# Optimization experiments

Hardware: AMD Instinct MI355X
Metric: run time of the kernel (lower is better)

## Reference

```python
import jax, jax.numpy as jnp
import numpy as np

H = 2048      # hidden_size
NH = 16       # num heads
HD = H // NH  # head_dim = 128


def setup_inputs() -> dict:
    key = jax.random.key(0)
    ks = jax.random.split(key, 5)
    x = jax.random.normal(ks[0], (2, 2048, H), dtype=jnp.float32)
    # qkv_proj: Linear(H, 3H) with bias; out_proj: Linear(H, H) with bias
    s = 1.0 / np.sqrt(H)
    w_qkv = jax.random.uniform(ks[1], (3 * H, H), jnp.float32, -s, s)
    b_qkv = jax.random.uniform(ks[2], (3 * H,), jnp.float32, -s, s)
    w_out = jax.random.uniform(ks[3], (H, H), jnp.float32, -s, s)
    b_out = jax.random.uniform(ks[4], (H,), jnp.float32, -s, s)
    return {"x": x, "w_qkv": w_qkv, "b_qkv": b_qkv, "w_out": w_out, "b_out": b_out}


def reference(x, w_qkv, b_qkv, w_out, b_out):
    b, s, _ = x.shape
    # fused QKV projection: [b, s, 3H]
    xqkv = jnp.einsum('bsh,oh->bso', x, w_qkv) + b_qkv
    xqkv = xqkv.reshape(b, s, 3, NH, HD)
    q = xqkv[:, :, 0].transpose(0, 2, 1, 3)  # [b, nh, s, hd]
    k = xqkv[:, :, 1].transpose(0, 2, 1, 3)
    v = xqkv[:, :, 2].transpose(0, 2, 1, 3)
    # non-causal SDPA (attn_mask=None, is_causal=False)
    scores = jnp.einsum('bhqd,bhkd->bhqk', q, k) / np.sqrt(HD).astype(np.float32)
    attn = jax.nn.softmax(scores, axis=-1)
    out = jnp.einsum('bhqk,bhkd->bhqd', attn, v)
    out = out.transpose(0, 2, 1, 3).reshape(b, s, NH * HD)
    return jnp.einsum('bsh,oh->bso', out, w_out) + b_out
```

## Files before the change

### kernel.cpp

```cpp
#include <hip/hip_runtime.h>
#include <hip/hip_bf16.h>


typedef __bf16 bf16x8 __attribute__((ext_vector_type(8)));
typedef float f32x4 __attribute__((ext_vector_type(4)));
typedef unsigned short ushort8_t __attribute__((ext_vector_type(8)));
typedef unsigned short ushort4_t __attribute__((ext_vector_type(4)));

__device__ __forceinline__ unsigned short f2bf(float f) {
  unsigned int u = __float_as_uint(f);
  u += 0x7fffu + ((u >> 16) & 1u);
  return (unsigned short)(u >> 16);
}

__device__ __forceinline__ unsigned int pk2bf(float lo, float hi) {
  unsigned int a = (__float_as_uint(lo) + 0x8000u) >> 16;
  unsigned int b = (__float_as_uint(hi) + 0x8000u) & 0xffff0000u;
  return a | b;
}

__device__ __forceinline__ float fexp2(float x) {
#if __has_builtin(__builtin_amdgcn_exp2f)
  return __builtin_amdgcn_exp2f(x);
#else
  return exp2f(x);
#endif
}

__device__ __forceinline__ f32x4 mfma16(bf16x8 a, bf16x8 b, f32x4 c) {
  return __builtin_amdgcn_mfma_f32_16x16x32_bf16(a, b, c, 0, 0, 0);
}

__device__ __forceinline__ void gload_lds16(const void* g, void* lds) {
  __builtin_amdgcn_global_load_lds(
      (const __attribute__((address_space(1))) unsigned int*)g,
      (__attribute__((address_space(3))) unsigned int*)lds, 16, 0, 0);
}

__global__ __launch_bounds__(256) void f32_to_bf16_k(const float* __restrict__ in,
                                                     unsigned short* __restrict__ out,
                                                     int n) {
  int i = (blockIdx.x * 256 + threadIdx.x) * 8;
  if (i >= n) return;
  float4 a = *(const float4*)(in + i);
  float4 b = *(const float4*)(in + i + 4);
  ushort8_t o;
  o[0] = f2bf(a.x); o[1] = f2bf(a.y); o[2] = f2bf(a.z); o[3] = f2bf(a.w);
  o[4] = f2bf(b.x); o[5] = f2bf(b.y); o[6] = f2bf(b.z); o[7] = f2bf(b.w);
  *(ushort8_t*)(out + i) = o;
}

template <int BF16OUT>
__global__ __launch_bounds__(256) void gemm_nt(const unsigned short* __restrict__ A,
                                               const unsigned short* __restrict__ B,
                                               const float* __restrict__ bias,
                                               void* __restrict__ Cout,
                                               int M, int N, int K) {
  __shared__ __attribute__((aligned(16))) unsigned short As[128 * 64];
  __shared__ __attribute__((aligned(16))) unsigned short Bs[128 * 64];
  const int tid = threadIdx.x;
  const int lane = tid & 63;
  const int wv = tid >> 6;
  const int wm = wv >> 1, wn = wv & 1;
  const int lr = lane & 15, lg = lane >> 4;
  const int m0 = blockIdx.y * 128, n0 = blockIdx.x * 128;

  f32x4 acc[4][4];
#pragma unroll
  for (int i = 0; i < 4; ++i)
#pragma unroll
    for (int j = 0; j < 4; ++j) acc[i][j] = (f32x4){0.f, 0.f, 0.f, 0.f};

  for (int kt = 0; kt < K; kt += 64) {
    __syncthreads();
#pragma unroll
    for (int i = 0; i < 4; ++i) {
      int c = i * 256 + tid;
      int r = c >> 3;
      int lc = (c & 7) ^ (r & 7);
      gload_lds16(A + (size_t)(m0 + r) * K + kt + lc * 8, &As[c * 8]);
      gload_lds16(B + (size_t)(n0 + r) * K + kt + lc * 8, &Bs[c * 8]);
    }
    __syncthreads();
#pragma unroll
    for (int kk = 0; kk < 64; kk += 32) {
      bf16x8 af[4], bf[4];
#pragma unroll
      for (int i = 0; i < 4; ++i) {
        int pcA = ((kk >> 3) + lg) ^ (lr & 7);
        af[i] = *(const bf16x8*)&As[(wm * 64 + i * 16 + lr) * 64 + pcA * 8];
        bf[i] = *(const bf16x8*)&Bs[(wn * 64 + i * 16 + lr) * 64 + pcA * 8];
      }
#pragma unroll
      for (int i = 0; i < 4; ++i)
#pragma unroll
        for (int j = 0; j < 4; ++j) acc[i][j] = mfma16(af[i], bf[j], acc[i][j]);
    }
  }

#pragma unroll
  for (int j = 0; j < 4; ++j) {
    int n = n0 + wn * 64 + j * 16 + lr;
    float bv = bias[n];
#pragma unroll
    for (int i = 0; i < 4; ++i) {
      int mbase = m0 + wm * 64 + i * 16 + lg * 4;
#pragma unroll
      for (int r = 0; r < 4; ++r) {
        float v = acc[i][j][r] + bv;
        if (BF16OUT)
          ((unsigned short*)Cout)[(size_t)(mbase + r) * N + n] = f2bf(v);
        else
          ((float*)Cout)[(size_t)(mbase + r) * N + n] = v;
      }
    }
  }
}

__global__ __launch_bounds__(256) void transpose_v(const unsigned short* __restrict__ qkv,
                                                   unsigned short* __restrict__ vT) {
  __shared__ __attribute__((aligned(16))) unsigned short T[64 * 128];
  const int tid = threadIdx.x;
  const int bh = blockIdx.y;
  const int b = bh >> 4, h = bh & 15;
  const int s0 = blockIdx.x * 64;
#pragma unroll
  for (int i = 0; i < 4; ++i) {
    int slot = i * 256 + tid;
    int s = slot >> 4;
    int lc = (slot & 15) ^ (s & 15);
    gload_lds16(qkv + (size_t)(b * 2048 + s0 + s) * 6144 + 4096 + h * 128 + lc * 8,
                &T[slot * 8]);
  }
  __syncthreads();
#pragma unroll
  for (int i = 0; i < 4; ++i) {
    int slot = i * 256 + tid;
    int d = slot >> 3, sc = slot & 7;
    ushort8_t v;
#pragma unroll
    for (int j = 0; j < 8; ++j) {
      int s = sc * 8 + j;
      v[j] = T[s * 128 + (((d >> 3) ^ (s & 15)) * 8) + (d & 7)];
    }
    *(ushort8_t*)&vT[((size_t)bh * 128 + d) * 2048 + s0 + sc * 8] = v;
  }
}

__global__ __launch_bounds__(256, 4) void flash_attn(const unsigned short* __restrict__ qkv,
                                                     const unsigned short* __restrict__ vT,
                                                     unsigned short* __restrict__ attnb) {
  __shared__ __attribute__((aligned(16))) unsigned short Ks[64 * 128];
  __shared__ __attribute__((aligned(16))) unsigned short Vt[128 * 64];

  const int tid = threadIdx.x;
  const int lane = tid & 63;
  const int w = tid >> 6;
  const int bh = blockIdx.y;
  const int b = bh >> 4, h = bh & 15;
  const int q0 = blockIdx.x * 64;
  const int lr = lane & 15, lg = lane >> 4;
  const float cs = 0.08838834764831845f * 1.44269504088896340f;

  bf16x8 qf[4];
  {
    int m = b * 2048 + q0 + w * 16 + lr;
    const unsigned short* qrow = qkv + (size_t)m * 6144 + h * 128;
#pragma unroll
    for (int kb = 0; kb < 4; ++kb) qf[kb] = *(const bf16x8*)(qrow + kb * 32 + lg * 8);
  }

  float l_i = 0.f;
  f32x4 O[8];
#pragma unroll
  for (int nb = 0; nb < 8; ++nb) O[nb] = (f32x4){0.f, 0.f, 0.f, 0.f};

  const unsigned short* vbase = vT + (size_t)bh * 128 * 2048;
  const int srcA = lr + ((lg & 1) ? 32 : 0);
  const int srcB = srcA + 16;
  const bool hi = (lg >> 1) != 0;

  for (int t = 0; t < 32; ++t) {
    const int s0k = t * 64;
    __syncthreads();
    const int krow = b * 2048 + s0k;
#pragma unroll
    for (int i = 0; i < 4; ++i) {
      int c = i * 256 + tid;
      int r = c >> 4;
      int lc = (c & 15) ^ (r & 15);
      gload_lds16(qkv + (size_t)(krow + r) * 6144 + 2048 + h * 128 + lc * 8, &Ks[c * 8]);
    }
#pragma unroll
    for (int i = 0; i < 4; ++i) {
      int c = i * 256 + tid;
      int r = c >> 3;
      int lc = (c & 7) ^ (r & 7);
      gload_lds16(vbase + (size_t)r * 2048 + s0k + lc * 8, &Vt[c * 8]);
    }
    __syncthreads();

    f32x4 sc[4];
#pragma unroll
    for (int cb = 0; cb < 4; ++cb) sc[cb] = (f32x4){0.f, 0.f, 0.f, 0.f};
#pragma unroll
    for (int cb = 0; cb < 4; ++cb) {
#pragma unroll
      for (int kb = 0; kb < 4; ++kb) {
        int pc = (kb * 4 + lg) ^ lr;
        bf16x8 kf = *(const bf16x8*)&Ks[(cb * 16 + lr) * 128 + pc * 8];
        sc[cb] = mfma16(kf, qf[kb], sc[cb]);
      }
    }

    float rs = 0.f;
    unsigned int pk[4][2];
#pragma unroll
    for (int cb = 0; cb < 4; ++cb) {
      float p0 = fexp2(sc[cb][0] * cs);
      float p1 = fexp2(sc[cb][1] * cs);
      float p2 = fexp2(sc[cb][2] * cs);
      float p3 = fexp2(sc[cb][3] * cs);
      rs += (p0 + p1) + (p2 + p3);
      pk[cb][0] = pk2bf(p0, p1);
      pk[cb][1] = pk2bf(p2, p3);
    }
    rs += __shfl_xor(rs, 16, 64);
    rs += __shfl_xor(rs, 32, 64);
    l_i += rs;

#pragma unroll
    for (int kb2 = 0; kb2 < 2; ++kb2) {
      unsigned int x0a = __shfl((int)pk[2 * kb2 + 0][0], srcA, 64);
      unsigned int x0b = __shfl((int)pk[2 * kb2 + 1][0], srcA, 64);
      unsigned int x1a = __shfl((int)pk[2 * kb2 + 0][1], srcA, 64);
      unsigned int x1b = __shfl((int)pk[2 * kb2 + 1][1], srcA, 64);
      unsigned int x2a = __shfl((int)pk[2 * kb2 + 0][0], srcB, 64);
      unsigned int x2b = __shfl((int)pk[2 * kb2 + 1][0], srcB, 64);
      unsigned int x3a = __shfl((int)pk[2 * kb2 + 0][1], srcB, 64);
      unsigned int x3b = __shfl((int)pk[2 * kb2 + 1][1], srcB, 64);
      uint4 u;
      u.x = hi ? x0b : x0a;
      u.y = hi ? x1b : x1a;
      u.z = hi ? x2b : x2a;
      u.w = hi ? x3b : x3a;
      bf16x8 pf = *(bf16x8*)&u;
#pragma unroll
      for (int nb = 0; nb < 8; ++nb) {
        int pc = (kb2 * 4 + lg) ^ (lr & 7);
        bf16x8 vtf = *(const bf16x8*)&Vt[(nb * 16 + lr) * 64 + pc * 8];
        O[nb] = mfma16(vtf, pf, O[nb]);
      }
    }
  }

  {
    int m = b * 2048 + q0 + w * 16 + lr;
    float inv = 1.0f / l_i;
    unsigned short* orow = attnb + (size_t)m * 2048 + h * 128;
#pragma unroll
    for (int nb = 0; nb < 8; ++nb) {
      ushort4_t o4;
#pragma unroll
      for (int r = 0; r < 4; ++r) o4[r] = f2bf(O[nb][r] * inv);
      *(ushort4_t*)&orow[nb * 16 + lg * 4] = o4;
    }
  }
}

extern "C" void kernel_launch(void* const* d_in, const int* in_sizes, int n_in,
                              void* d_out, int out_size, void* d_ws, size_t ws_size,
                              hipStream_t stream) {
  const float* x = (const float*)d_in[0];
  const float* w_qkv = (const float*)d_in[1];
  const float* b_qkv = (const float*)d_in[2];
  const float* w_out = (const float*)d_in[3];
  const float* b_out = (const float*)d_in[4];
  float* out = (float*)d_out;

  char* ws = (char*)d_ws;
  unsigned short* xb = (unsigned short*)ws;
  unsigned short* attnb = xb;
  unsigned short* wqkvb = (unsigned short*)(ws + (16u << 20));
  unsigned short* woutb = wqkvb;
  unsigned short* qkvb = (unsigned short*)(ws + (40u << 20));
  unsigned short* vT = (unsigned short*)(ws + (88u << 20));

  f32_to_bf16_k<<<8388608 / 2048, 256, 0, stream>>>(x, xb, 8388608);
  f32_to_bf16_k<<<12582912 / 2048, 256, 0, stream>>>(w_qkv, wqkvb, 12582912);

  gemm_nt<1><<<dim3(48, 32), 256, 0, stream>>>(xb, wqkvb, b_qkv, qkvb, 4096, 6144, 2048);

  f32_to_bf16_k<<<4194304 / 2048, 256, 0, stream>>>(w_out, woutb, 4194304);
  transpose_v<<<dim3(32, 32), 256, 0, stream>>>(qkvb, vT);

  flash_attn<<<dim3(32, 32), 256, 0, stream>>>(qkvb, vT, attnb);

  gemm_nt<0><<<dim3(16, 32), 256, 0, stream>>>(attnb, woutb, b_out, out, 4096, 2048, 2048);
}
```

Measured before the change: 429.1 us.

## Double-buffer K/V tiles in flash attention and fuse V transpose into GEMM epilogue

The flash attention kernel now keeps two K/V tile buffers in LDS, so it can prefetch the next tile with async global-to-LDS loads while computing on the current one. That halves the barriers per tile. The price is double the shared memory, with occupancy lowered to 2 blocks per SIMD. Separately, the QKV GEMM is split in two: one launch writes Q/K row-major, and another writes V directly in transposed per-head layout from its epilogue. This removes the standalone transpose_v kernel and its extra pass over V. The transposed epilogue writes 4-element strided chunks, which may coalesce worse.

```diff
diff --git a/kernel.cpp b/kernel.cpp
--- a/kernel.cpp
+++ b/kernel.cpp
@@ -50,12 +50,12 @@
   *(ushort8_t*)(out + i) = o;
 }
 
-template <int BF16OUT>
+template <int OUT_MODE>
 __global__ __launch_bounds__(256) void gemm_nt(const unsigned short* __restrict__ A,
                                                const unsigned short* __restrict__ B,
                                                const float* __restrict__ bias,
                                                void* __restrict__ Cout,
-                                               int M, int N, int K) {
+                                               int Ns, int K) {
   __shared__ __attribute__((aligned(16))) unsigned short As[128 * 64];
   __shared__ __attribute__((aligned(16))) unsigned short Bs[128 * 64];
   const int tid = threadIdx.x;
@@ -105,53 +105,34 @@
 #pragma unroll
     for (int i = 0; i < 4; ++i) {
       int mbase = m0 + wm * 64 + i * 16 + lg * 4;
-#pragma unroll
-      for (int r = 0; r < 4; ++r) {
-        float v = acc[i][j][r] + bv;
-        if (BF16OUT)
-          ((unsigned short*)Cout)[(size_t)(mbase + r) * N + n] = f2bf(v);
-        else
-          ((float*)Cout)[(size_t)(mbase + r) * N + n] = v;
+      if (OUT_MODE == 2) {
+        int hh = n >> 7, dd = n & 127;
+        int b = mbase >> 11, s = mbase & 2047;
+        ushort4_t o4;
+#pragma unroll
+        for (int r = 0; r < 4; ++r) o4[r] = f2bf(acc[i][j][r] + bv);
+        *(ushort4_t*)&((unsigned short*)Cout)[((size_t)((b * 16 + hh) * 128 + dd)) * 2048 + s] = o4;
+      } else {
+#pragma unroll
+        for (int r = 0; r < 4; ++r) {
+          float v = acc[i][j][r] + bv;
+          if (OUT_MODE == 1)
+            ((unsigned short*)Cout)[(size_t)(mbase + r) * Ns + n] = f2bf(v);
+          else
+            ((float*)Cout)[(size_t)(mbase + r) * Ns + n] = v;
+        }
       }
     }
   }
 }
 
-__global__ __launch_bounds__(256) void transpose_v(const unsigned short* __restrict__ qkv,
-                                                   unsigned short* __restrict__ vT) {
-  __shared__ __attribute__((aligned(16))) unsigned short T[64 * 128];
-  const int tid = threadIdx.x;
-  const int bh = blockIdx.y;
-  const int b = bh >> 4, h = bh & 15;
-  const int s0 = blockIdx.x * 64;
-#pragma unroll
-  for (int i = 0; i < 4; ++i) {
-    int slot = i * 256 + tid;
-    int s = slot >> 4;
-    int lc = (slot & 15) ^ (s & 15);
-    gload_lds16(qkv + (size_t)(b * 2048 + s0 + s) * 6144 + 4096 + h * 128 + lc * 8,
-                &T[slot * 8]);
-  }
-  __syncthreads();
-#pragma unroll
-  for (int i = 0; i < 4; ++i) {
-    int slot = i * 256 + tid;
-    int d = slot >> 3, sc = slot & 7;
-    ushort8_t v;
-#pragma unroll
-    for (int j = 0; j < 8; ++j) {
-      int s = sc * 8 + j;
-      v[j] = T[s * 128 + (((d >> 3) ^ (s & 15)) * 8) + (d & 7)];
-    }
-    *(ushort8_t*)&vT[((size_t)bh * 128 + d) * 2048 + s0 + sc * 8] = v;
-  }
-}
-
-__global__ __launch_bounds__(256, 4) void flash_attn(const unsigned short* __restrict__ qkv,
+__global__ __launch_bounds__(256, 2) void flash_attn(const unsigned short* __restrict__ qkv,
                                                      const unsigned short* __restrict__ vT,
                                                      unsigned short* __restrict__ attnb) {
-  __shared__ __attribute__((aligned(16))) unsigned short Ks[64 * 128];
-  __shared__ __attribute__((aligned(16))) unsigned short Vt[128 * 64];
+  __shared__ __attribute__((aligned(16))) unsigned short Ks0[64 * 128];
+  __shared__ __attribute__((aligned(16))) unsigned short Ks1[64 * 128];
+  __shared__ __attribute__((aligned(16))) unsigned short Vt0[128 * 64];
+  __shared__ __attribute__((aligned(16))) unsigned short Vt1[128 * 64];
 
   const int tid = threadIdx.x;
   const int lane = tid & 63;
@@ -180,79 +161,94 @@
   const int srcB = srcA + 16;
   const bool hi = (lg >> 1) != 0;
 
-  for (int t = 0; t < 32; ++t) {
-    const int s0k = t * 64;
-    __syncthreads();
-    const int krow = b * 2048 + s0k;
-#pragma unroll
-    for (int i = 0; i < 4; ++i) {
-      int c = i * 256 + tid;
-      int r = c >> 4;
-      int lc = (c & 15) ^ (r & 15);
-      gload_lds16(qkv + (size_t)(krow + r) * 6144 + 2048 + h * 128 + lc * 8, &Ks[c * 8]);
-    }
-#pragma unroll
-    for (int i = 0; i < 4; ++i) {
-      int c = i * 256 + tid;
-      int r = c >> 3;
-      int lc = (c & 7) ^ (r & 7);
-      gload_lds16(vbase + (size_t)r * 2048 + s0k + lc * 8, &Vt[c * 8]);
-    }
-    __syncthreads();
-
-    f32x4 sc[4];
-#pragma unroll
-    for (int cb = 0; cb < 4; ++cb) sc[cb] = (f32x4){0.f, 0.f, 0.f, 0.f};
-#pragma unroll
-    for (int cb = 0; cb < 4; ++cb) {
-#pragma unroll
-      for (int kb = 0; kb < 4; ++kb) {
-        int pc = (kb * 4 + lg) ^ lr;
-        bf16x8 kf = *(const bf16x8*)&Ks[(cb * 16 + lr) * 128 + pc * 8];
-        sc[cb] = mfma16(kf, qf[kb], sc[cb]);
-      }
-    }
-
-    float rs = 0.f;
-    unsigned int pk[4][2];
-#pragma unroll
-    for (int cb = 0; cb < 4; ++cb) {
-      float p0 = fexp2(sc[cb][0] * cs);
-      float p1 = fexp2(sc[cb][1] * cs);
-      float p2 = fexp2(sc[cb][2] * cs);
-      float p3 = fexp2(sc[cb][3] * cs);
-      rs += (p0 + p1) + (p2 + p3);
-      pk[cb][0] = pk2bf(p0, p1);
-      pk[cb][1] = pk2bf(p2, p3);
-    }
-    rs += __shfl_xor(rs, 16, 64);
-    rs += __shfl_xor(rs, 32, 64);
-    l_i += rs;
-
-#pragma unroll
-    for (int kb2 = 0; kb2 < 2; ++kb2) {
-      unsigned int x0a = __shfl((int)pk[2 * kb2 + 0][0], srcA, 64);
-      unsigned int x0b = __shfl((int)pk[2 * kb2 + 1][0], srcA, 64);
-      unsigned int x1a = __shfl((int)pk[2 * kb2 + 0][1], srcA, 64);
-      unsigned int x1b = __shfl((int)pk[2 * kb2 + 1][1], srcA, 64);
-      unsigned int x2a = __shfl((int)pk[2 * kb2 + 0][0], srcB, 64);
-      unsigned int x2b = __shfl((int)pk[2 * kb2 + 1][0], srcB, 64);
-      unsigned int x3a = __shfl((int)pk[2 * kb2 + 0][1], srcB, 64);
-      unsigned int x3b = __shfl((int)pk[2 * kb2 + 1][1], srcB, 64);
-      uint4 u;
-      u.x = hi ? x0b : x0a;
-      u.y = hi ? x1b : x1a;
-      u.z = hi ? x2b : x2a;
-      u.w = hi ? x3b : x3a;
-      bf16x8 pf = *(bf16x8*)&u;
-#pragma unroll
-      for (int nb = 0; nb < 8; ++nb) {
-        int pc = (kb2 * 4 + lg) ^ (lr & 7);
-        bf16x8 vtf = *(const bf16x8*)&Vt[(nb * 16 + lr) * 64 + pc * 8];
-        O[nb] = mfma16(vtf, pf, O[nb]);
-      }
-    }
-  }
+#define STAGE(KS, VT, T_) do {                                                          \
+    int s0k_ = (T_) * 64;                                                               \
+    int krow_ = b * 2048 + s0k_;                                                        \
+    _Pragma("unroll")                                                                   \
+    for (int i_ = 0; i_ < 4; ++i_) {                                                    \
+      int c_ = i_ * 256 + tid;                                                          \
+      int r_ = c_ >> 4;                                                                 \
+      int lc_ = (c_ & 15) ^ (r_ & 15);                                                  \
+      gload_lds16(qkv + (size_t)(krow_ + r_) * 6144 + 2048 + h * 128 + lc_ * 8,         \
+                  &KS[c_ * 8]);                                                         \
+    }                                                                                   \
+    _Pragma("unroll")                                                                   \
+    for (int i_ = 0; i_ < 4; ++i_) {                                                    \
+      int c_ = i_ * 256 + tid;                                                          \
+      int r_ = c_ >> 3;                                                                 \
+      int lc_ = (c_ & 7) ^ (r_ & 7);                                                    \
+      gload_lds16(vbase + (size_t)r_ * 2048 + s0k_ + lc_ * 8, &VT[c_ * 8]);             \
+    }                                                                                   \
+  } while (0)
+
+#define COMPUTE(KS, VT) do {                                                            \
+    f32x4 sc[4];                                                                        \
+    _Pragma("unroll")                                                                   \
+    for (int cb = 0; cb < 4; ++cb) sc[cb] = (f32x4){0.f, 0.f, 0.f, 0.f};                \
+    _Pragma("unroll")                                                                   \
+    for (int cb = 0; cb < 4; ++cb) {                                                    \
+      _Pragma("unroll")                                                                 \
+      for (int kb = 0; kb < 4; ++kb) {                                                  \
+        int pc = (kb * 4 + lg) ^ lr;                                                    \
+        bf16x8 kf = *(const bf16x8*)&KS[(cb * 16 + lr) * 128 + pc * 8];                 \
+        sc[cb] = mfma16(kf, qf[kb], sc[cb]);                                            \
+      }                                                                                 \
+    }                                                                                   \
+    float rs = 0.f;                                                                     \
+    unsigned int pk[4][2];                                                              \
+    _Pragma("unroll")                                                                   \
+    for (int cb = 0; cb < 4; ++cb) {                                                    \
+      float p0 = fexp2(sc[cb][0] * cs);                                                 \
+      float p1 = fexp2(sc[cb][1] * cs);                                                 \
+      float p2 = fexp2(sc[cb][2] * cs);                                                 \
+      float p3 = fexp2(sc[cb][3] * cs);                                                 \
+      rs += (p0 + p1) + (p2 + p3);                                                      \
+      pk[cb][0] = pk2bf(p0, p1);                                                        \
+      pk[cb][1] = pk2bf(p2, p3);                                                        \
+    }                                                                                   \
+    rs += __shfl_xor(rs, 16, 64);                                                       \
+    rs += __shfl_xor(rs, 32, 64);                                                       \
+    l_i += rs;                                                                          \
+    _Pragma("unroll")                                                                   \
+    for (int kb2 = 0; kb2 < 2; ++kb2) {                                                 \
+      unsigned int x0a = __shfl((int)pk[2 * kb2 + 0][0], srcA, 64);                     \
+      unsigned int x0b = __shfl((int)pk[2 * kb2 + 1][0], srcA, 64);                     \
+      unsigned int x1a = __shfl((int)pk[2 * kb2 + 0][1], srcA, 64);                     \
+      unsigned int x1b = __shfl((int)pk[2 * kb2 + 1][1], srcA, 64);                     \
+      unsigned int x2a = __shfl((int)pk[2 * kb2 + 0][0], srcB, 64);                     \
+      unsigned int x2b = __shfl((int)pk[2 * kb2 + 1][0], srcB, 64);                     \
+      unsigned int x3a = __shfl((int)pk[2 * kb2 + 0][1], srcB, 64);                     \
+      unsigned int x3b = __shfl((int)pk[2 * kb2 + 1][1], srcB, 64);                     \
+      uint4 u;                                                                          \
+      u.x = hi ? x0b : x0a;                                                             \
+      u.y = hi ? x1b : x1a;                                                             \
+      u.z = hi ? x2b : x2a;                                                             \
+      u.w = hi ? x3b : x3a;                                                             \
+      bf16x8 pf = *(bf16x8*)&u;                                                         \
+      _Pragma("unroll")                                                                 \
+      for (int nb = 0; nb < 8; ++nb) {                                                  \
+        int pc = (kb2 * 4 + lg) ^ (lr & 7);                                             \
+        bf16x8 vtf = *(const bf16x8*)&VT[(nb * 16 + lr) * 64 + pc * 8];                 \
+        O[nb] = mfma16(vtf, pf, O[nb]);                                                 \
+      }                                                                                 \
+    }                                                                                   \
+  } while (0)
+
+  STAGE(Ks0, Vt0, 0);
+  __syncthreads();
+#pragma unroll 1
+  for (int pr = 0; pr < 16; ++pr) {
+    STAGE(Ks1, Vt1, 2 * pr + 1);
+    COMPUTE(Ks0, Vt0);
+    __syncthreads();
+    int nt = 2 * pr + 2;
+    if (nt > 31) nt = 31;
+    STAGE(Ks0, Vt0, nt);
+    COMPUTE(Ks1, Vt1);
+    __syncthreads();
+  }
+#undef STAGE
+#undef COMPUTE
 
   {
     int m = b * 2048 + q0 + w * 16 + lr;
@@ -289,12 +285,13 @@
   f32_to_bf16_k<<<8388608 / 2048, 256, 0, stream>>>(x, xb, 8388608);
   f32_to_bf16_k<<<12582912 / 2048, 256, 0, stream>>>(w_qkv, wqkvb, 12582912);
 
-  gemm_nt<1><<<dim3(48, 32), 256, 0, stream>>>(xb, wqkvb, b_qkv, qkvb, 4096, 6144, 2048);
+  gemm_nt<1><<<dim3(32, 32), 256, 0, stream>>>(xb, wqkvb, b_qkv, qkvb, 6144, 2048);
+  gemm_nt<2><<<dim3(16, 32), 256, 0, stream>>>(xb, wqkvb + (size_t)4096 * 2048,
+                                               b_qkv + 4096, vT, 2048, 2048);
 
   f32_to_bf16_k<<<4194304 / 2048, 256, 0, stream>>>(w_out, woutb, 4194304);
-  transpose_v<<<dim3(32, 32), 256, 0, stream>>>(qkvb, vT);
 
   flash_attn<<<dim3(32, 32), 256, 0, stream>>>(qkvb, vT, attnb);
 
-  gemm_nt<0><<<dim3(16, 32), 256, 0, stream>>>(attnb, woutb, b_out, out, 4096, 2048, 2048);
-}
+  gemm_nt<0><<<dim3(16, 32), 256, 0, stream>>>(attnb, woutb, b_out, out, 2048, 2048);
+}
```

Measured after the change: 439.2 us. 1.02x slower.

## Fuse V transpose into QKV GEMM epilogue and double query rows per attention block

Applied to the files above, without the earlier changes.

The QKV projection is split into two launches. The Q/K part writes the row-major buffer as before. The V part writes bf16 output directly in transposed [b,h,d,s] layout, which removes the separate transpose kernel and its read/write round trip. Flash attention now handles 128 query rows per block (two 16-row groups per wave), so each K/V tile loaded into LDS is reused across twice the queries, at the cost of more registers and lower occupancy (launch bounds change from 4 to 2). The Q/K GEMM keeps a row stride of 6144 while only computing the first 4096 columns.

```diff
diff --git a/kernel.cpp b/kernel.cpp
--- a/kernel.cpp
+++ b/kernel.cpp
@@ -50,12 +50,12 @@
   *(ushort8_t*)(out + i) = o;
 }
 
-template <int BF16OUT>
+template <int OUT_MODE>
 __global__ __launch_bounds__(256) void gemm_nt(const unsigned short* __restrict__ A,
                                                const unsigned short* __restrict__ B,
                                                const float* __restrict__ bias,
                                                void* __restrict__ Cout,
-                                               int M, int N, int K) {
+                                               int Ns, int K) {
   __shared__ __attribute__((aligned(16))) unsigned short As[128 * 64];
   __shared__ __attribute__((aligned(16))) unsigned short Bs[128 * 64];
   const int tid = threadIdx.x;
@@ -105,49 +105,28 @@
 #pragma unroll
     for (int i = 0; i < 4; ++i) {
       int mbase = m0 + wm * 64 + i * 16 + lg * 4;
-#pragma unroll
-      for (int r = 0; r < 4; ++r) {
-        float v = acc[i][j][r] + bv;
-        if (BF16OUT)
-          ((unsigned short*)Cout)[(size_t)(mbase + r) * N + n] = f2bf(v);
-        else
-          ((float*)Cout)[(size_t)(mbase + r) * N + n] = v;
-      }
-    }
-  }
-}
-
-__global__ __launch_bounds__(256) void transpose_v(const unsigned short* __restrict__ qkv,
-                                                   unsigned short* __restrict__ vT) {
-  __shared__ __attribute__((aligned(16))) unsigned short T[64 * 128];
-  const int tid = threadIdx.x;
-  const int bh = blockIdx.y;
-  const int b = bh >> 4, h = bh & 15;
-  const int s0 = blockIdx.x * 64;
-#pragma unroll
-  for (int i = 0; i < 4; ++i) {
-    int slot = i * 256 + tid;
-    int s = slot >> 4;
-    int lc = (slot & 15) ^ (s & 15);
-    gload_lds16(qkv + (size_t)(b * 2048 + s0 + s) * 6144 + 4096 + h * 128 + lc * 8,
-                &T[slot * 8]);
-  }
-  __syncthreads();
-#pragma unroll
-  for (int i = 0; i < 4; ++i) {
-    int slot = i * 256 + tid;
-    int d = slot >> 3, sc = slot & 7;
-    ushort8_t v;
-#pragma unroll
-    for (int j = 0; j < 8; ++j) {
-      int s = sc * 8 + j;
-      v[j] = T[s * 128 + (((d >> 3) ^ (s & 15)) * 8) + (d & 7)];
-    }
-    *(ushort8_t*)&vT[((size_t)bh * 128 + d) * 2048 + s0 + sc * 8] = v;
-  }
-}
-
-__global__ __launch_bounds__(256, 4) void flash_attn(const unsigned short* __restrict__ qkv,
+      if (OUT_MODE == 2) {
+        int hh = n >> 7, dd = n & 127;
+        int b = mbase >> 11, s = mbase & 2047;
+        ushort4_t o4;
+#pragma unroll
+        for (int r = 0; r < 4; ++r) o4[r] = f2bf(acc[i][j][r] + bv);
+        *(ushort4_t*)&((unsigned short*)Cout)[((size_t)((b * 16 + hh) * 128 + dd)) * 2048 + s] = o4;
+      } else {
+#pragma unroll
+        for (int r = 0; r < 4; ++r) {
+          float v = acc[i][j][r] + bv;
+          if (OUT_MODE == 1)
+            ((unsigned short*)Cout)[(size_t)(mbase + r) * Ns + n] = f2bf(v);
+          else
+            ((float*)Cout)[(size_t)(mbase + r) * Ns + n] = v;
+        }
+      }
+    }
+  }
+}
+
+__global__ __launch_bounds__(256, 2) void flash_attn(const unsigned short* __restrict__ qkv,
                                                      const unsigned short* __restrict__ vT,
                                                      unsigned short* __restrict__ attnb) {
   __shared__ __attribute__((aligned(16))) unsigned short Ks[64 * 128];
@@ -158,22 +137,25 @@
   const int w = tid >> 6;
   const int bh = blockIdx.y;
   const int b = bh >> 4, h = bh & 15;
-  const int q0 = blockIdx.x * 64;
+  const int q0 = blockIdx.x * 128;
   const int lr = lane & 15, lg = lane >> 4;
   const float cs = 0.08838834764831845f * 1.44269504088896340f;
 
-  bf16x8 qf[4];
-  {
-    int m = b * 2048 + q0 + w * 16 + lr;
+  bf16x8 qf[2][4];
+#pragma unroll
+  for (int g = 0; g < 2; ++g) {
+    int m = b * 2048 + q0 + w * 32 + g * 16 + lr;
     const unsigned short* qrow = qkv + (size_t)m * 6144 + h * 128;
 #pragma unroll
-    for (int kb = 0; kb < 4; ++kb) qf[kb] = *(const bf16x8*)(qrow + kb * 32 + lg * 8);
-  }
-
-  float l_i = 0.f;
-  f32x4 O[8];
-#pragma unroll
-  for (int nb = 0; nb < 8; ++nb) O[nb] = (f32x4){0.f, 0.f, 0.f, 0.f};
+    for (int kb = 0; kb < 4; ++kb) qf[g][kb] = *(const bf16x8*)(qrow + kb * 32 + lg * 8);
+  }
+
+  float l_i[2] = {0.f, 0.f};
+  f32x4 O[2][8];
+#pragma unroll
+  for (int g = 0; g < 2; ++g)
+#pragma unroll
+    for (int nb = 0; nb < 8; ++nb) O[g][nb] = (f32x4){0.f, 0.f, 0.f, 0.f};
 
   const unsigned short* vbase = vT + (size_t)bh * 128 * 2048;
   const int srcA = lr + ((lg & 1) ? 32 : 0);
@@ -200,69 +182,81 @@
     }
     __syncthreads();
 
-    f32x4 sc[4];
-#pragma unroll
-    for (int cb = 0; cb < 4; ++cb) sc[cb] = (f32x4){0.f, 0.f, 0.f, 0.f};
+    f32x4 sc[2][4];
+#pragma unroll
+    for (int g = 0; g < 2; ++g)
+#pragma unroll
+      for (int cb = 0; cb < 4; ++cb) sc[g][cb] = (f32x4){0.f, 0.f, 0.f, 0.f};
 #pragma unroll
     for (int cb = 0; cb < 4; ++cb) {
 #pragma unroll
       for (int kb = 0; kb < 4; ++kb) {
         int pc = (kb * 4 + lg) ^ lr;
         bf16x8 kf = *(const bf16x8*)&Ks[(cb * 16 + lr) * 128 + pc * 8];
-        sc[cb] = mfma16(kf, qf[kb], sc[cb]);
-      }
-    }
-
-    float rs = 0.f;
-    unsigned int pk[4][2];
-#pragma unroll
-    for (int cb = 0; cb < 4; ++cb) {
-      float p0 = fexp2(sc[cb][0] * cs);
-      float p1 = fexp2(sc[cb][1] * cs);
-      float p2 = fexp2(sc[cb][2] * cs);
-      float p3 = fexp2(sc[cb][3] * cs);
-      rs += (p0 + p1) + (p2 + p3);
-      pk[cb][0] = pk2bf(p0, p1);
-      pk[cb][1] = pk2bf(p2, p3);
-    }
-    rs += __shfl_xor(rs, 16, 64);
-    rs += __shfl_xor(rs, 32, 64);
-    l_i += rs;
+        sc[0][cb] = mfma16(kf, qf[0][kb], sc[0][cb]);
+        sc[1][cb] = mfma16(kf, qf[1][kb], sc[1][cb]);
+      }
+    }
+
+    unsigned int pk[2][4][2];
+#pragma unroll
+    for (int g = 0; g < 2; ++g) {
+      float rs = 0.f;
+#pragma unroll
+      for (int cb = 0; cb < 4; ++cb) {
+        float p0 = fexp2(sc[g][cb][0] * cs);
+        float p1 = fexp2(sc[g][cb][1] * cs);
+        float p2 = fexp2(sc[g][cb][2] * cs);
+        float p3 = fexp2(sc[g][cb][3] * cs);
+        rs += (p0 + p1) + (p2 + p3);
+        pk[g][cb][0] = pk2bf(p0, p1);
+        pk[g][cb][1] = pk2bf(p2, p3);
+      }
+      rs += __shfl_xor(rs, 16, 64);
+      rs += __shfl_xor(rs, 32, 64);
+      l_i[g] += rs;
+    }
 
 #pragma unroll
     for (int kb2 = 0; kb2 < 2; ++kb2) {
-      unsigned int x0a = __shfl((int)pk[2 * kb2 + 0][0], srcA, 64);
-      unsigned int x0b = __shfl((int)pk[2 * kb2 + 1][0], srcA, 64);
-      unsigned int x1a = __shfl((int)pk[2 * kb2 + 0][1], srcA, 64);
-      unsigned int x1b = __shfl((int)pk[2 * kb2 + 1][1], srcA, 64);
-      unsigned int x2a = __shfl((int)pk[2 * kb2 + 0][0], srcB, 64);
-      unsigned int x2b = __shfl((int)pk[2 * kb2 + 1][0], srcB, 64);
-      unsigned int x3a = __shfl((int)pk[2 * kb2 + 0][1], srcB, 64);
-      unsigned int x3b = __shfl((int)pk[2 * kb2 + 1][1], srcB, 64);
-      uint4 u;
-      u.x = hi ? x0b : x0a;
-      u.y = hi ? x1b : x1a;
-      u.z = hi ? x2b : x2a;
-      u.w = hi ? x3b : x3a;
-      bf16x8 pf = *(bf16x8*)&u;
+      bf16x8 pf[2];
+#pragma unroll
+      for (int g = 0; g < 2; ++g) {
+        unsigned int x0a = __shfl((int)pk[g][2 * kb2 + 0][0], srcA, 64);
+        unsigned int x0b = __shfl((int)pk[g][2 * kb2 + 1][0], srcA, 64);
+        unsigned int x1a = __shfl((int)pk[g][2 * kb2 + 0][1], srcA, 64);
+        unsigned int x1b = __shfl((int)pk[g][2 * kb2 + 1][1], srcA, 64);
+        unsigned int x2a = __shfl((int)pk[g][2 * kb2 + 0][0], srcB, 64);
+        unsigned int x2b = __shfl((int)pk[g][2 * kb2 + 1][0], srcB, 64);
+        unsigned int x3a = __shfl((int)pk[g][2 * kb2 + 0][1], srcB, 64);
+        unsigned int x3b = __shfl((int)pk[g][2 * kb2 + 1][1], srcB, 64);
+        uint4 u;
+        u.x = hi ? x0b : x0a;
+        u.y = hi ? x1b : x1a;
+        u.z = hi ? x2b : x2a;
+        u.w = hi ? x3b : x3a;
+        pf[g] = *(bf16x8*)&u;
+      }
 #pragma unroll
       for (int nb = 0; nb < 8; ++nb) {
         int pc = (kb2 * 4 + lg) ^ (lr & 7);
         bf16x8 vtf = *(const bf16x8*)&Vt[(nb * 16 + lr) * 64 + pc * 8];
-        O[nb] = mfma16(vtf, pf, O[nb]);
-      }
-    }
-  }
-
-  {
-    int m = b * 2048 + q0 + w * 16 + lr;
-    float inv = 1.0f / l_i;
+        O[0][nb] = mfma16(vtf, pf[0], O[0][nb]);
+        O[1][nb] = mfma16(vtf, pf[1], O[1][nb]);
+      }
+    }
+  }
+
+#pragma unroll
+  for (int g = 0; g < 2; ++g) {
+    int m = b * 2048 + q0 + w * 32 + g * 16 + lr;
+    float inv = 1.0f / l_i[g];
     unsigned short* orow = attnb + (size_t)m * 2048 + h * 128;
 #pragma unroll
     for (int nb = 0; nb < 8; ++nb) {
       ushort4_t o4;
 #pragma unroll
-      for (int r = 0; r < 4; ++r) o4[r] = f2bf(O[nb][r] * inv);
+      for (int r = 0; r < 4; ++r) o4[r] = f2bf(O[g][nb][r] * inv);
       *(ushort4_t*)&orow[nb * 16 + lg * 4] = o4;
     }
   }
@@ -289,12 +283,13 @@
   f32_to_bf16_k<<<8388608 / 2048, 256, 0, stream>>>(x, xb, 8388608);
   f32_to_bf16_k<<<12582912 / 2048, 256, 0, stream>>>(w_qkv, wqkvb, 12582912);
 
-  gemm_nt<1><<<dim3(48, 32), 256, 0, stream>>>(xb, wqkvb, b_qkv, qkvb, 4096, 6144, 2048);
+  gemm_nt<1><<<dim3(32, 32), 256, 0, stream>>>(xb, wqkvb, b_qkv, qkvb, 6144, 2048);
+  gemm_nt<2><<<dim3(16, 32), 256, 0, stream>>>(xb, wqkvb + (size_t)4096 * 2048,
+                                               b_qkv + 4096, vT, 2048, 2048);
 
   f32_to_bf16_k<<<4194304 / 2048, 256, 0, stream>>>(w_out, woutb, 4194304);
-  transpose_v<<<dim3(32, 32), 256, 0, stream>>>(qkvb, vT);
-
-  flash_attn<<<dim3(32, 32), 256, 0, stream>>>(qkvb, vT, attnb);
-
-  gemm_nt<0><<<dim3(16, 32), 256, 0, stream>>>(attnb, woutb, b_out, out, 4096, 2048, 2048);
-}
+
+  flash_attn<<<dim3(16, 32), 256, 0, stream>>>(qkvb, vT, attnb);
+
+  gemm_nt<0><<<dim3(16, 32), 256, 0, stream>>>(attnb, woutb, b_out, out, 2048, 2048);
+}
```

Result: faster. 404.1 us (-5.8%).
